# Kernel optimization log

Measured on AMD Instinct MI355X. Metric: run time of the kernel, lower is better.

Reference implementation:

```python
import jax, jax.numpy as jnp
import numpy as np


def setup_inputs() -> dict:
    key = jax.random.key(0)
    k1, k2 = jax.random.split(key)
    bz, c, h, w = 8, 512, 64, 64
    x = jax.random.normal(k1, (bz, c, h, w), dtype=jnp.float32)
    # binary mask over spatial positions; flag is its flattened view (must be consistent)
    mask = jax.random.randint(k2, (h, w), 0, 2, dtype=jnp.int32)
    flag = mask.reshape(-1)
    return {"input": x, "mask": mask, "flag": flag,
            "shift_sz": 1, "stride": 1, "triple_w": 1}


def reference(input, mask, flag, shift_sz, stride, triple_w):
    # input: [B, C, H, W]; former = first C/2 channels (decoder feats),
    # latter = last C/2 channels (encoder feats). shift_sz=stride=1 -> 1x1 patches,
    # i.e. per-pixel feature vectors.
    bz, c, h, w = input.shape
    ch = c // 2
    S = h * w
    former = input[:, :ch]                      # [B, ch, H, W]
    latter = input[:, ch:]                      # [B, ch, H, W]

    f = former.reshape(bz, ch, S).transpose(0, 2, 1)   # [B, S, ch] query pixels
    l = latter.reshape(bz, ch, S).transpose(0, 2, 1)   # [B, S, ch] key pixels

    # _norm: L2-normalize latter patches (rows)
    l_norm = l / jnp.maximum(jnp.linalg.norm(l, axis=-1, keepdims=True), 1e-12)

    # cosine-style similarity between every former pixel and every latter pixel
    sim = jnp.einsum('bqc,bkc->bqk', f, l_norm)        # [B, S, S]

    # only non-masked (flag==0) latter pixels are valid match candidates
    neg = jnp.asarray(-1e30, sim.dtype)
    sim = jnp.where((flag == 0)[None, None, :], sim, neg)
    idx = jnp.argmax(sim, axis=-1)                     # [B, S] nearest-neighbor index

    # gather matched latter pixels; paste only at masked (flag==1) positions,
    # zero elsewhere (masked_fill_(inv_ex_mask, 0) zeroes the non-mask region)
    shifted = jnp.take_along_axis(l, idx[..., None], axis=1)       # [B, S, ch]
    shifted = jnp.where((flag == 1)[None, :, None], shifted, 0.0)
    shifted = shifted.transpose(0, 2, 1).reshape(bz, ch, h, w)

    return jnp.concatenate([former, latter, shifted], axis=1)       # [B, 3*ch, H, W]
```

## Files before the change

kernel.cpp:

```cpp
#include <hip/hip_runtime.h>

#define S    4096
#define CH   256
#define NB   8

#define BM   128
#define BN   64
#define KSPLIT 8

#define SFF  256.0f
#define SLL  1024.0f

#define NEG_INF (-3.402823466e38f)

typedef _Float16 half8 __attribute__((ext_vector_type(8)));
typedef float    f32x4 __attribute__((ext_vector_type(4)));

__global__ void compact(const int* __restrict__ flag, int* __restrict__ cnts,
                        int* __restrict__ qlist, int* __restrict__ klist,
                        int* __restrict__ qpos,  int* __restrict__ kpos) {
    __shared__ int sq[256], sk[256];
    int t = threadIdx.x;
    int base = t * 16;
    int f[16];
    int nq = 0, nk = 0;
    #pragma unroll
    for (int i = 0; i < 16; ++i) {
        f[i] = flag[base + i];
        nq += (f[i] == 1);
        nk += (f[i] == 0);
    }
    sq[t] = nq; sk[t] = nk;
    __syncthreads();
    for (int off = 1; off < 256; off <<= 1) {
        int vq = sq[t], vk = sk[t];
        int aq = (t >= off) ? sq[t - off] : 0;
        int ak = (t >= off) ? sk[t - off] : 0;
        __syncthreads();
        sq[t] = vq + aq; sk[t] = vk + ak;
        __syncthreads();
    }
    int pq = sq[t] - nq;
    int pk = sk[t] - nk;
    #pragma unroll
    for (int i = 0; i < 16; ++i) {
        if (f[i] == 1) { qpos[base + i] = pq; qlist[pq++] = base + i; }
        else           { kpos[base + i] = pk; klist[pk++] = base + i; }
    }
    if (t == 255) { cnts[0] = sq[255]; cnts[1] = sk[255]; }
}

__global__ void pack_both(const float* __restrict__ x, const int* __restrict__ flag,
                          const int* __restrict__ qpos, const int* __restrict__ kpos,
                          float* __restrict__ out) {
    __shared__ float T[16][257];
    const int b = blockIdx.z;
    const int t = threadIdx.x;
    const int s = blockIdx.x * 256 + t;

    if (blockIdx.y < 4) {
        const int c0b = blockIdx.y * 64;
        const float* src = x + (size_t)b * 512 * S + blockIdx.x * 256;
        const bool active = (flag[s] == 1);
        const int row = active ? qpos[s] : 0;
        half8* F2 = (half8*)(out + (size_t)b * 768 * S);
        const int g  = row >> 4;
        const int sr = row & 15;
        for (int c0 = c0b; c0 < c0b + 64; c0 += 16) {
            #pragma unroll
            for (int i = 0; i < 16; ++i)
                T[i][t] = src[(size_t)(c0 + i) * S + t];
            __syncthreads();
            if (active) {
                #pragma unroll
                for (int g8 = 0; g8 < 2; ++g8) {
                    const int c  = c0 + g8 * 8;
                    const int cc = c >> 5;
                    const int l4 = (c >> 3) & 3;
                    half8 hb, lb;
                    #pragma unroll
                    for (int j = 0; j < 8; ++j) {
                        float v = T[g8 * 8 + j][t] * SFF;
                        _Float16 h = (_Float16)v;
                        hb[j] = h;
                        lb[j] = (_Float16)(v - (float)h);
                    }
                    F2[(size_t)(((g * 2 + 0) * 8 + cc) * 64) + sr * 4 + l4] = hb;
                    F2[(size_t)(((g * 2 + 1) * 8 + cc) * 64) + sr * 4 + l4] = lb;
                }
            }
            __syncthreads();
        }
    } else {
        const float* src = x + ((size_t)b * 512 + 256) * S + blockIdx.x * 256;
        const bool active = (flag[s] == 0);
        const int row = active ? kpos[s] : 0;
        _Float16* LH = (_Float16*)(out + (size_t)b * 768 * S) + 2 * (size_t)S * CH;
        _Float16* LL = LH + (size_t)S * CH;

        float acc = 0.f;
        for (int c0 = 0; c0 < CH; c0 += 16) {
            #pragma unroll
            for (int i = 0; i < 16; ++i)
                T[i][t] = src[(size_t)(c0 + i) * S + t];
            __syncthreads();
            #pragma unroll
            for (int i = 0; i < 16; ++i) {
                float v = T[i][t];
                acc += v * v;
            }
            __syncthreads();
        }
        const float w = active ? (1.0f / fmaxf(sqrtf(acc), 1e-12f)) * SLL : 0.f;

        for (int c0 = 0; c0 < CH; c0 += 16) {
            #pragma unroll
            for (int i = 0; i < 16; ++i)
                T[i][t] = src[(size_t)(c0 + i) * S + t];
            __syncthreads();
            if (active) {
                #pragma unroll
                for (int g8 = 0; g8 < 2; ++g8) {
                    union { _Float16 u[8]; float4 v; } hb, lb;
                    #pragma unroll
                    for (int j = 0; j < 8; ++j) {
                        float v = T[g8 * 8 + j][t] * w;
                        _Float16 h = (_Float16)v;
                        hb.u[j] = h;
                        lb.u[j] = (_Float16)(v - (float)h);
                    }
                    *(float4*)&LH[(size_t)row * CH + c0 + g8 * 8] = hb.v;
                    *(float4*)&LL[(size_t)row * CH + c0 + g8 * 8] = lb.v;
                }
            }
            __syncthreads();
        }
    }
}

__global__ void zero_pad(const int* __restrict__ cnts, float* __restrict__ out) {
    const int b  = blockIdx.y;
    const int Aq = cnts[0], Ak = cnts[1];
    const int aqp = (Aq + BM - 1) & ~(BM - 1);
    const int akp = (Ak + BN - 1) & ~(BN - 1);
    _Float16* pb = (_Float16*)(out + (size_t)b * 768 * S);
    int i = blockIdx.x * 256 + threadIdx.x;
    half8 z = { 0, 0, 0, 0, 0, 0, 0, 0 };
    if (i < 8192) {
        int p = i >> 12, rem = i & 4095;
        int row = Aq + (rem >> 5);
        int sl  = rem & 31;
        if (row < aqp) {
            half8* F2 = (half8*)pb;
            F2[(size_t)((((row >> 4) * 2 + p) * 8 + (sl >> 2)) * 64) + (row & 15) * 4 + (sl & 3)] = z;
        }
    } else {
        int j = i - 8192, panel = j >> 11, jdx = j & 2047;
        int row = Ak + (jdx >> 5);
        if (row < akp)
            *(half8*)(pb + (size_t)(2 + panel) * S * CH + (size_t)row * CH + (jdx & 31) * 8) = z;
    }
}

#define MFMA(A, B, C) __builtin_amdgcn_mfma_f32_16x16x32_f16((A), (B), (C), 0, 0, 0)

#define GLDS(SRC, OFF) __builtin_amdgcn_global_load_lds( \
    (const __attribute__((address_space(1))) void*)(SRC), \
    (__attribute__((address_space(3))) void*)(lds + (OFF)), 16, 0, 0)

#define STAGE(OFF) do { GLDS(s4, (OFF) + woff); GLDS(s5, (OFF) + 4096 + woff); } while (0)

#define ADV() do { \
    if (tn + 1 < nchunk) { \
        if ((tn & 7) == 7) { s4 += 32320; s5 += 32320; } \
        else               { s4 += 64;    s5 += 64;    } \
    } \
    ++tn; \
} while (0)

#define FOLD() do { \
    _Pragma("unroll") \
    for (int nt = 0; nt < 4; ++nt) { \
        int kp = kpb + nt * 16; \
        if (kp < Ak) { \
            _Pragma("unroll") \
            for (int mt = 0; mt < 2; ++mt) { \
                _Pragma("unroll") \
                for (int r = 0; r < 4; ++r) { \
                    const int ix = mt * 4 + r; \
                    float sv = acc[mt][nt][r]; \
                    if (sv > rm[ix]) { rm[ix] = sv; ri[ix] = kp; } \
                } \
            } \
        } \
        acc[0][nt] = (f32x4){0.f, 0.f, 0.f, 0.f}; \
        acc[1][nt] = (f32x4){0.f, 0.f, 0.f, 0.f}; \
    } \
    kpb += 64; \
} while (0)

#define CBODY(BASE, CC) do { \
    const char* _bb = lds + (BASE); \
    half8 bh0 = *(const half8*)(_bb + boff_h[0]); \
    half8 bl0 = *(const half8*)(_bb + boff_l[0]); \
    half8 bh1 = *(const half8*)(_bb + boff_h[1]); \
    half8 bl1 = *(const half8*)(_bb + boff_l[1]); \
    half8 bh2 = *(const half8*)(_bb + boff_h[2]); \
    half8 bl2 = *(const half8*)(_bb + boff_l[2]); \
    half8 bh3 = *(const half8*)(_bb + boff_h[3]); \
    half8 bl3 = *(const half8*)(_bb + boff_l[3]); \
    acc[0][0] = MFMA(ah0[CC], bh0, acc[0][0]); \
    acc[1][0] = MFMA(ah1[CC], bh0, acc[1][0]); \
    acc[0][0] = MFMA(ah0[CC], bl0, acc[0][0]); \
    acc[1][0] = MFMA(ah1[CC], bl0, acc[1][0]); \
    acc[0][0] = MFMA(al0[CC], bh0, acc[0][0]); \
    acc[1][0] = MFMA(al1[CC], bh0, acc[1][0]); \
    acc[0][1] = MFMA(ah0[CC], bh1, acc[0][1]); \
    acc[1][1] = MFMA(ah1[CC], bh1, acc[1][1]); \
    acc[0][1] = MFMA(ah0[CC], bl1, acc[0][1]); \
    acc[1][1] = MFMA(ah1[CC], bl1, acc[1][1]); \
    acc[0][1] = MFMA(al0[CC], bh1, acc[0][1]); \
    acc[1][1] = MFMA(al1[CC], bh1, acc[1][1]); \
    acc[0][2] = MFMA(ah0[CC], bh2, acc[0][2]); \
    acc[1][2] = MFMA(ah1[CC], bh2, acc[1][2]); \
    acc[0][2] = MFMA(ah0[CC], bl2, acc[0][2]); \
    acc[1][2] = MFMA(ah1[CC], bl2, acc[1][2]); \
    acc[0][2] = MFMA(al0[CC], bh2, acc[0][2]); \
    acc[1][2] = MFMA(al1[CC], bh2, acc[1][2]); \
    acc[0][3] = MFMA(ah0[CC], bh3, acc[0][3]); \
    acc[1][3] = MFMA(ah1[CC], bh3, acc[1][3]); \
    acc[0][3] = MFMA(ah0[CC], bl3, acc[0][3]); \
    acc[1][3] = MFMA(ah1[CC], bl3, acc[1][3]); \
    acc[0][3] = MFMA(al0[CC], bh3, acc[0][3]); \
    acc[1][3] = MFMA(al1[CC], bh3, acc[1][3]); \
} while (0)

#define PHASE(J) do { \
    asm volatile("s_waitcnt vmcnt(4)" ::: "memory"); \
    __builtin_amdgcn_s_barrier(); \
    STAGE(sto); ADV(); \
    STAGE(sto + 8192); ADV(); \
    __builtin_amdgcn_s_setprio(1); \
    CBODY(rdo,        2 * (J)); \
    CBODY(rdo + 8192, 2 * (J) + 1); \
    __builtin_amdgcn_s_setprio(0); \
    rdo = (rdo == 32768) ? 0 : rdo + 16384; \
    sto = (sto == 32768) ? 0 : sto + 16384; \
} while (0)

__launch_bounds__(256)
__global__ void argmax_mfma(const float* __restrict__ outbuf,
                            const int*  __restrict__ cnts,
                            float* __restrict__ pmax,
                            int*   __restrict__ pidx) {
    __shared__ __align__(1024) char lds[6 * 8192];

    const int Aq    = cnts[0];
    const int Ak    = cnts[1];
    const int b     = blockIdx.y;
    const int split = blockIdx.x & (KSPLIT - 1);
    const int q0    = (blockIdx.x >> 3) * BM;
    if (q0 >= Aq) return;

    const int tid  = threadIdx.x;
    const int lane = tid & 63;
    const int wid  = tid >> 6;
    const int l15  = lane & 15;
    const int l4   = lane >> 4;
    const int woff = wid * 1024;

    const _Float16* pb  = (const _Float16*)(outbuf + (size_t)b * 768 * S);
    const _Float16* LHg = pb + 2 * (size_t)S * CH;
    const _Float16* LLg = pb + 3 * (size_t)S * CH;

    const int nkt = (Ak + BN - 1) / BN;
    const int kt0 = (nkt * split) / KSPLIT;
    const int kt1 = (nkt * (split + 1)) / KSPLIT;
    const int nchunk = (kt1 - kt0) * 8;

    float rm[8]; int ri[8];
    #pragma unroll
    for (int i = 0; i < 8; ++i) { rm[i] = NEG_INF; ri[i] = 0; }

    int boff_h[4], boff_l[4];
    #pragma unroll
    for (int nt = 0; nt < 4; ++nt) {
        int rowb = nt * 16 + l15;
        int swzb = (rowb & 7) << 4;
        boff_h[nt] = rowb * 128 + ((l4 * 16)        ^ swzb);
        boff_l[nt] = rowb * 128 + (((l4 * 16) + 64) ^ swzb);
    }

    if (nchunk > 0) {
        half8 ah0[8], al0[8], ah1[8], al1[8];
        {
            const half8* F2 = (const half8*)pb;
            const int g0 = (q0 >> 4) + wid * 2;
            const int lo = l15 * 4 + l4;
            #pragma unroll
            for (int cc = 0; cc < 8; ++cc) {
                ah0[cc] = F2[(size_t)((((g0    ) * 2 + 0) * 8 + cc) * 64) + lo];
                al0[cc] = F2[(size_t)((((g0    ) * 2 + 1) * 8 + cc) * 64) + lo];
                ah1[cc] = F2[(size_t)((((g0 + 1) * 2 + 0) * 8 + cc) * 64) + lo];
                al1[cc] = F2[(size_t)((((g0 + 1) * 2 + 1) * 8 + cc) * 64) + lo];
            }
        }

        const char *s4, *s5;
        {
            #define LSRC(P) ({ int s_ = (P) * 256 + tid; int row_ = s_ >> 3; \
                int ls_ = (s_ & 7) ^ (row_ & 7); \
                (const char*)(((ls_ < 4) ? LHg : LLg) + (size_t)(kt0 * BN + row_) * CH + (ls_ & 3) * 8); })
            s4 = LSRC(0); s5 = LSRC(1);
            #undef LSRC
        }
        int tn = 0;

        f32x4 acc[2][4];
        #pragma unroll
        for (int mt = 0; mt < 2; ++mt)
            #pragma unroll
            for (int nt = 0; nt < 4; ++nt) acc[mt][nt] = (f32x4){0.f, 0.f, 0.f, 0.f};

        int kpb = kt0 * BN + l15;

        STAGE(0);     ADV();
        STAGE(8192);  ADV();
        STAGE(16384); ADV();
        STAGE(24576); ADV();

        int rdo = 0;
        int sto = 32768;
        const int ngroup = kt1 - kt0;
        for (int g = 0; g < ngroup; ++g) {
            PHASE(0);
            PHASE(1);
            PHASE(2);
            PHASE(3);
            FOLD();
        }
    }

    #pragma unroll
    for (int mt = 0; mt < 2; ++mt) {
        #pragma unroll
        for (int r = 0; r < 4; ++r) {
            const int ix = mt * 4 + r;
            float m = rm[ix]; int id = ri[ix];
            #pragma unroll
            for (int off = 8; off; off >>= 1) {
                float om = __shfl_xor(m, off, 64);
                int   oi = __shfl_xor(id, off, 64);
                if (om > m || (om == m && oi < id)) { m = om; id = oi; }
            }
            if (l15 == 0) {
                int qp = q0 + wid * 32 + mt * 16 + l4 * 4 + r;
                if (qp < Aq) {
                    size_t o = ((size_t)((b << 12) + qp)) * KSPLIT + split;
                    pmax[o] = m;
                    pidx[o] = id;
                }
            }
        }
    }
}

__global__ void combine(const int* __restrict__ cnts, const int* __restrict__ qlist,
                        const int* __restrict__ klist,
                        const float* __restrict__ pmax, const int* __restrict__ pidx,
                        int* __restrict__ idxb) {
    int qp = blockIdx.x * 256 + threadIdx.x;
    int b  = blockIdx.y;
    if (qp >= cnts[0]) return;
    size_t base = (size_t)((b << 12) + qp) * KSPLIT;
    float m = pmax[base]; int id = pidx[base];
    #pragma unroll
    for (int s = 1; s < KSPLIT; ++s) {
        float om = pmax[base + s]; int oi = pidx[base + s];
        if (om > m) { m = om; id = oi; }
    }
    idxb[((size_t)b << 12) + qlist[qp]] = klist[id];
}

__global__ void writeback(const float* __restrict__ x, const int* __restrict__ flag,
                          const int* __restrict__ idxb, float* __restrict__ out) {
    int i = blockIdx.x * 256 + threadIdx.x;
    int b = blockIdx.y;
    int c = i >> 10;
    float4* dst = (float4*)(out + (size_t)b * 768 * S) + i;
    if (c < 512) {
        *dst = ((const float4*)(x + (size_t)b * 512 * S))[i];
    } else {
        const float* src = x + ((size_t)b * 512 + 256 + (c - 512)) * S;
        const int* ib = idxb + ((size_t)b << 12);
        int q = (i & 1023) * 4;
        float4 v = { 0.f, 0.f, 0.f, 0.f };
        if (flag[q + 0] == 1) v.x = src[ib[q + 0]];
        if (flag[q + 1] == 1) v.y = src[ib[q + 1]];
        if (flag[q + 2] == 1) v.z = src[ib[q + 2]];
        if (flag[q + 3] == 1) v.w = src[ib[q + 3]];
        *dst = v;
    }
}

extern "C" void kernel_launch(void* const* d_in, const int* in_sizes, int n_in,
                              void* d_out, int out_size, void* d_ws, size_t ws_size,
                              hipStream_t stream) {
    const float* x    = (const float*)d_in[0];
    const int*   flag = (const int*)d_in[2];
    float*       out  = (float*)d_out;

    char* ws = (char*)d_ws;
    int*   cnts  = (int*)(ws);
    int*   qlist = (int*)(ws + 1024);
    int*   klist = (int*)(ws + 17408);
    int*   qpos  = (int*)(ws + 33792);
    int*   kpos  = (int*)(ws + 50176);
    int*   idxb  = (int*)(ws + 66560);
    float* pmax  = (float*)(ws + 197632);
    int*   pidx  = (int*)(ws + 1246208);

    hipLaunchKernelGGL(compact,     dim3(1),                     dim3(256), 0, stream, flag, cnts, qlist, klist, qpos, kpos);
    hipLaunchKernelGGL(pack_both,   dim3(S / 256, 5, NB),        dim3(256), 0, stream, x, flag, qpos, kpos, out);
    hipLaunchKernelGGL(zero_pad,    dim3(48, NB),                dim3(256), 0, stream, cnts, out);
    hipLaunchKernelGGL(argmax_mfma, dim3((S / BM) * KSPLIT, NB), dim3(256), 0, stream, out, cnts, pmax, pidx);
    hipLaunchKernelGGL(combine,     dim3(S / 256, NB),           dim3(256), 0, stream, cnts, qlist, klist, pmax, pidx, idxb);
    hipLaunchKernelGGL(writeback,   dim3(768 * 1024 / 256, NB),  dim3(256), 0, stream, x, flag, idxb, out);
}
```

Baseline: 163.1 us.

## Halve query tile to 64 rows with one 16-row MFMA tile per wave

Shrinks the block's query tile from 128 to 64 rows, so each wave holds A fragments for a single 16-row group instead of two. Accumulators, running-max state and A registers are halved, and the B offsets become a single base plus constant strides. This aims to cut register pressure and raise occupancy or the number of blocks. The cost is that each LDS-staged key tile is reused across half as many queries, doubling global/LDS traffic per FLOP.

```diff
diff --git a/kernel.cpp b/kernel.cpp
--- a/kernel.cpp
+++ b/kernel.cpp
@@ -4,7 +4,7 @@
 #define CH   256
 #define NB   8
 
-#define BM   128
+#define BM   64
 #define BN   64
 #define KSPLIT 8
 
@@ -184,55 +184,39 @@
         int kp = kpb + nt * 16; \
         if (kp < Ak) { \
             _Pragma("unroll") \
-            for (int mt = 0; mt < 2; ++mt) { \
-                _Pragma("unroll") \
-                for (int r = 0; r < 4; ++r) { \
-                    const int ix = mt * 4 + r; \
-                    float sv = acc[mt][nt][r]; \
-                    if (sv > rm[ix]) { rm[ix] = sv; ri[ix] = kp; } \
-                } \
+            for (int r = 0; r < 4; ++r) { \
+                float sv = acc[nt][r]; \
+                if (sv > rm[r]) { rm[r] = sv; ri[r] = kp; } \
             } \
         } \
-        acc[0][nt] = (f32x4){0.f, 0.f, 0.f, 0.f}; \
-        acc[1][nt] = (f32x4){0.f, 0.f, 0.f, 0.f}; \
+        acc[nt] = (f32x4){0.f, 0.f, 0.f, 0.f}; \
     } \
     kpb += 64; \
 } while (0)
 
 #define CBODY(BASE, CC) do { \
-    const char* _bb = lds + (BASE); \
-    half8 bh0 = *(const half8*)(_bb + boff_h[0]); \
-    half8 bl0 = *(const half8*)(_bb + boff_l[0]); \
-    half8 bh1 = *(const half8*)(_bb + boff_h[1]); \
-    half8 bl1 = *(const half8*)(_bb + boff_l[1]); \
-    half8 bh2 = *(const half8*)(_bb + boff_h[2]); \
-    half8 bl2 = *(const half8*)(_bb + boff_l[2]); \
-    half8 bh3 = *(const half8*)(_bb + boff_h[3]); \
-    half8 bl3 = *(const half8*)(_bb + boff_l[3]); \
-    acc[0][0] = MFMA(ah0[CC], bh0, acc[0][0]); \
-    acc[1][0] = MFMA(ah1[CC], bh0, acc[1][0]); \
-    acc[0][0] = MFMA(ah0[CC], bl0, acc[0][0]); \
-    acc[1][0] = MFMA(ah1[CC], bl0, acc[1][0]); \
-    acc[0][0] = MFMA(al0[CC], bh0, acc[0][0]); \
-    acc[1][0] = MFMA(al1[CC], bh0, acc[1][0]); \
-    acc[0][1] = MFMA(ah0[CC], bh1, acc[0][1]); \
-    acc[1][1] = MFMA(ah1[CC], bh1, acc[1][1]); \
-    acc[0][1] = MFMA(ah0[CC], bl1, acc[0][1]); \
-    acc[1][1] = MFMA(ah1[CC], bl1, acc[1][1]); \
-    acc[0][1] = MFMA(al0[CC], bh1, acc[0][1]); \
-    acc[1][1] = MFMA(al1[CC], bh1, acc[1][1]); \
-    acc[0][2] = MFMA(ah0[CC], bh2, acc[0][2]); \
-    acc[1][2] = MFMA(ah1[CC], bh2, acc[1][2]); \
-    acc[0][2] = MFMA(ah0[CC], bl2, acc[0][2]); \
-    acc[1][2] = MFMA(ah1[CC], bl2, acc[1][2]); \
-    acc[0][2] = MFMA(al0[CC], bh2, acc[0][2]); \
-    acc[1][2] = MFMA(al1[CC], bh2, acc[1][2]); \
-    acc[0][3] = MFMA(ah0[CC], bh3, acc[0][3]); \
-    acc[1][3] = MFMA(ah1[CC], bh3, acc[1][3]); \
-    acc[0][3] = MFMA(ah0[CC], bl3, acc[0][3]); \
-    acc[1][3] = MFMA(ah1[CC], bl3, acc[1][3]); \
-    acc[0][3] = MFMA(al0[CC], bh3, acc[0][3]); \
-    acc[1][3] = MFMA(al1[CC], bh3, acc[1][3]); \
+    const char* _bh = lds + (BASE) + boff0h; \
+    const char* _bl = lds + (BASE) + boff0l; \
+    half8 bh0 = *(const half8*)(_bh); \
+    half8 bl0 = *(const half8*)(_bl); \
+    half8 bh1 = *(const half8*)(_bh + 2048); \
+    half8 bl1 = *(const half8*)(_bl + 2048); \
+    half8 bh2 = *(const half8*)(_bh + 4096); \
+    half8 bl2 = *(const half8*)(_bl + 4096); \
+    half8 bh3 = *(const half8*)(_bh + 6144); \
+    half8 bl3 = *(const half8*)(_bl + 6144); \
+    acc[0] = MFMA(ah[CC], bh0, acc[0]); \
+    acc[1] = MFMA(ah[CC], bh1, acc[1]); \
+    acc[2] = MFMA(ah[CC], bh2, acc[2]); \
+    acc[3] = MFMA(ah[CC], bh3, acc[3]); \
+    acc[0] = MFMA(ah[CC], bl0, acc[0]); \
+    acc[1] = MFMA(ah[CC], bl1, acc[1]); \
+    acc[2] = MFMA(ah[CC], bl2, acc[2]); \
+    acc[3] = MFMA(ah[CC], bl3, acc[3]); \
+    acc[0] = MFMA(al[CC], bh0, acc[0]); \
+    acc[1] = MFMA(al[CC], bh1, acc[1]); \
+    acc[2] = MFMA(al[CC], bh2, acc[2]); \
+    acc[3] = MFMA(al[CC], bh3, acc[3]); \
 } while (0)
 
 #define PHASE(J) do { \
@@ -278,31 +262,23 @@
     const int kt1 = (nkt * (split + 1)) / KSPLIT;
     const int nchunk = (kt1 - kt0) * 8;
 
-    float rm[8]; int ri[8];
-    #pragma unroll
-    for (int i = 0; i < 8; ++i) { rm[i] = NEG_INF; ri[i] = 0; }
-
-    int boff_h[4], boff_l[4];
-    #pragma unroll
-    for (int nt = 0; nt < 4; ++nt) {
-        int rowb = nt * 16 + l15;
-        int swzb = (rowb & 7) << 4;
-        boff_h[nt] = rowb * 128 + ((l4 * 16)        ^ swzb);
-        boff_l[nt] = rowb * 128 + (((l4 * 16) + 64) ^ swzb);
-    }
+    float rm[4]; int ri[4];
+    #pragma unroll
+    for (int i = 0; i < 4; ++i) { rm[i] = NEG_INF; ri[i] = 0; }
+
+    const int boff0h = l15 * 128 + ((l4 * 16) ^ ((l15 & 7) << 4));
+    const int boff0l = boff0h ^ 64;
 
     if (nchunk > 0) {
-        half8 ah0[8], al0[8], ah1[8], al1[8];
+        half8 ah[8], al[8];
         {
             const half8* F2 = (const half8*)pb;
-            const int g0 = (q0 >> 4) + wid * 2;
+            const int g0 = (q0 >> 4) + wid;
             const int lo = l15 * 4 + l4;
             #pragma unroll
             for (int cc = 0; cc < 8; ++cc) {
-                ah0[cc] = F2[(size_t)((((g0    ) * 2 + 0) * 8 + cc) * 64) + lo];
-                al0[cc] = F2[(size_t)((((g0    ) * 2 + 1) * 8 + cc) * 64) + lo];
-                ah1[cc] = F2[(size_t)((((g0 + 1) * 2 + 0) * 8 + cc) * 64) + lo];
-                al1[cc] = F2[(size_t)((((g0 + 1) * 2 + 1) * 8 + cc) * 64) + lo];
+                ah[cc] = F2[(size_t)(((g0 * 2 + 0) * 8 + cc) * 64) + lo];
+                al[cc] = F2[(size_t)(((g0 * 2 + 1) * 8 + cc) * 64) + lo];
             }
         }
 
@@ -316,11 +292,9 @@
         }
         int tn = 0;
 
-        f32x4 acc[2][4];
+        f32x4 acc[4];
         #pragma unroll
-        for (int mt = 0; mt < 2; ++mt)
-            #pragma unroll
-            for (int nt = 0; nt < 4; ++nt) acc[mt][nt] = (f32x4){0.f, 0.f, 0.f, 0.f};
+        for (int nt = 0; nt < 4; ++nt) acc[nt] = (f32x4){0.f, 0.f, 0.f, 0.f};
 
         int kpb = kt0 * BN + l15;
 
@@ -342,24 +316,20 @@
     }
 
     #pragma unroll
-    for (int mt = 0; mt < 2; ++mt) {
+    for (int r = 0; r < 4; ++r) {
+        float m = rm[r]; int id = ri[r];
         #pragma unroll
-        for (int r = 0; r < 4; ++r) {
-            const int ix = mt * 4 + r;
-            float m = rm[ix]; int id = ri[ix];
-            #pragma unroll
-            for (int off = 8; off; off >>= 1) {
-                float om = __shfl_xor(m, off, 64);
-                int   oi = __shfl_xor(id, off, 64);
-                if (om > m || (om == m && oi < id)) { m = om; id = oi; }
-            }
-            if (l15 == 0) {
-                int qp = q0 + wid * 32 + mt * 16 + l4 * 4 + r;
-                if (qp < Aq) {
-                    size_t o = ((size_t)((b << 12) + qp)) * KSPLIT + split;
-                    pmax[o] = m;
-                    pidx[o] = id;
-                }
+        for (int off = 8; off; off >>= 1) {
+            float om = __shfl_xor(m, off, 64);
+            int   oi = __shfl_xor(id, off, 64);
+            if (om > m || (om == m && oi < id)) { m = om; id = oi; }
+        }
+        if (l15 == 0) {
+            int qp = q0 + wid * 16 + l4 * 4 + r;
+            if (qp < Aq) {
+                size_t o = ((size_t)((b << 12) + qp)) * KSPLIT + split;
+                pmax[o] = m;
+                pidx[o] = id;
             }
         }
     }
```

Measured after the change: 158.3 us. -2.9%, faster.
